# Kernel optimization log

Hardware: AMD Instinct MI355X
Metric: run time of the kernel (lower is better)

Reference implementation:

```python
import jax, jax.numpy as jnp
import numpy as np

EMBED_DIM = 768
NUM_HEADS = 12
HEAD_DIM = EMBED_DIM // NUM_HEADS
SCALE = HEAD_DIM ** -0.5


def setup_inputs() -> dict:
    key = jax.random.key(0)
    k_x, k_qw, k_qb, k_pw, k_pb = jax.random.split(key, 5)
    B, N, C = 8, 1024, EMBED_DIM
    std = C ** -0.5
    return {
        "x": jax.random.normal(k_x, (B, N, C), dtype=jnp.float32),
        "qkv_w": jax.random.normal(k_qw, (C, 3 * C), dtype=jnp.float32) * std,
        "qkv_b": jax.random.normal(k_qb, (3 * C,), dtype=jnp.float32) * 0.02,
        "proj_w": jax.random.normal(k_pw, (C, C), dtype=jnp.float32) * std,
        "proj_b": jax.random.normal(k_pb, (C,), dtype=jnp.float32) * 0.02,
    }


def reference(x, qkv_w, qkv_b, proj_w, proj_b):
    B, N, C = x.shape
    # QKV projection: [B,N,3C] -> [3,B,H,N,Dh]
    qkv = (x @ qkv_w + qkv_b).reshape(B, N, 3, NUM_HEADS, HEAD_DIM)
    qkv = jnp.transpose(qkv, (2, 0, 3, 1, 4))
    q, k, v = qkv[0], qkv[1], qkv[2]
    # attention scores [B,H,N,N]
    attn = jnp.einsum("bhqd,bhkd->bhqk", q, k) * SCALE
    attn_weights = jax.nn.softmax(attn, axis=-1)
    # dropout=0.0 (eval) -> identity
    out = jnp.einsum("bhqk,bhkd->bhqd", attn_weights, v)
    out = jnp.transpose(out, (0, 2, 1, 3)).reshape(B, N, C)
    out = out @ proj_w + proj_b
    return out, attn_weights
```

## Files before the change

### kernel.cpp

```cpp
#include <hip/hip_runtime.h>
#include <cstdint>
#include <cstddef>

namespace {

constexpr int B = 8, NSEQ = 1024, C = 768, H = 12, D = 64, N3 = 2304;
constexpr float SCALE = 0.125f;
constexpr size_t QKV_ELEMS = (size_t)B * H * NSEQ * D;

using f32x4 = __attribute__((ext_vector_type(4))) float;
using s16x8 = __attribute__((ext_vector_type(8))) short;

__device__ __forceinline__ unsigned short f2bf(float f) {
  union { float f; uint32_t u; } v; v.f = f;
  const uint32_t r = v.u + 0x7FFFu + ((v.u >> 16) & 1u);
  return (unsigned short)(r >> 16);
}
__device__ __forceinline__ float bf2f(unsigned short s) {
  union { uint32_t u; float f; } v; v.u = ((uint32_t)s) << 16;
  return v.f;
}
__device__ __forceinline__ void gload_lds16(const void* g, void* l) {
  __builtin_amdgcn_global_load_lds(
      (const __attribute__((address_space(1))) uint32_t*)g,
      (__attribute__((address_space(3))) uint32_t*)l, 16, 0, 0);
}

__global__ __launch_bounds__(256)
void cvt_x(const float* __restrict__ x, unsigned short* __restrict__ xb, int n4) {
  const int stride = gridDim.x * 256;
  for (int idx = blockIdx.x * 256 + threadIdx.x; idx < n4; idx += stride) {
    const float4 v = ((const float4*)x)[idx];
    ushort4 o;
    o.x = f2bf(v.x); o.y = f2bf(v.y); o.z = f2bf(v.z); o.w = f2bf(v.w);
    ((ushort4*)xb)[idx] = o;
  }
}

__global__ __launch_bounds__(256)
void transp_cvt(const float* __restrict__ w, unsigned short* __restrict__ wt,
                int K, int N) {
  __shared__ float t[32][33];
  const int n0 = blockIdx.x << 5, k0 = blockIdx.y << 5;
  const int tid = threadIdx.x;
  #pragma unroll
  for (int r = 0; r < 4; ++r) {
    const int e = (r << 8) + tid;
    const int kk = e >> 5, nn = e & 31;
    t[kk][nn] = w[(size_t)(k0 + kk) * N + n0 + nn];
  }
  __syncthreads();
  #pragma unroll
  for (int r = 0; r < 4; ++r) {
    const int e = (r << 8) + tid;
    const int nn = e >> 5, kk = e & 31;
    wt[(size_t)(n0 + nn) * K + k0 + kk] = f2bf(t[kk][nn]);
  }
}

template<int MODE>
__global__ __launch_bounds__(256, 2)
void gemm_bf16(const unsigned short* __restrict__ A,
               const unsigned short* __restrict__ Wt,
               const float* __restrict__ bias,
               unsigned short* __restrict__ qp, unsigned short* __restrict__ kp,
               unsigned short* __restrict__ vt, float* __restrict__ out32,
               int N, int NT) {
  constexpr int K = 768;
  __shared__ short As[128 * 64];
  __shared__ short Bs[128 * 64];
  const int tid = threadIdx.x;
  const int wid = tid >> 6, lane = tid & 63;
  const int wm = wid >> 1, wn = wid & 1;
  const int lg = lane >> 4, lr = lane & 15;

  const int cpx = gridDim.x >> 3;
  const int logical = (blockIdx.x & 7) * cpx + (blockIdx.x >> 3);
  const int bx = logical % NT, by = logical / NT;
  const int m0 = by << 7, n0 = bx << 7;

  f32x4 acc[4][4] = {};

  for (int k0 = 0; k0 < K; k0 += 64) {
    __syncthreads();
    #pragma unroll
    for (int r = 0; r < 4; ++r) {
      const int c = (r << 8) + tid;
      const int row = c >> 3, g8 = c & 7;
      const int gp = g8 ^ (row & 7);
      const int ldsoff = (((r << 8) + (wid << 6)) << 3);
      gload_lds16(A + (size_t)(m0 + row) * K + k0 + (gp << 3), (void*)(As + ldsoff));
      gload_lds16(Wt + (size_t)(n0 + row) * K + k0 + (gp << 3), (void*)(Bs + ldsoff));
    }
    __syncthreads();
    #pragma unroll
    for (int kc = 0; kc < 2; ++kc) {
      s16x8 af[4], bf[4];
      #pragma unroll
      for (int i = 0; i < 4; ++i) {
        const int ra = (wm << 6) + (i << 4) + lr;
        const int ca = ((kc << 2) + lg) ^ (ra & 7);
        af[i] = *(const s16x8*)(As + (ra << 6) + (ca << 3));
        const int rb = (wn << 6) + (i << 4) + lr;
        const int cb = ((kc << 2) + lg) ^ (rb & 7);
        bf[i] = *(const s16x8*)(Bs + (rb << 6) + (cb << 3));
      }
      #pragma unroll
      for (int i = 0; i < 4; ++i)
        #pragma unroll
        for (int j = 0; j < 4; ++j)
          acc[i][j] = __builtin_amdgcn_mfma_f32_16x16x32_bf16(af[i], bf[j], acc[i][j], 0, 0, 0);
    }
  }

  #pragma unroll
  for (int i = 0; i < 4; ++i) {
    const int m = m0 + (wm << 6) + (i << 4) + (lg << 2);
    #pragma unroll
    for (int j = 0; j < 4; ++j) {
      const int n = n0 + (wn << 6) + (j << 4) + lr;
      const float bv = bias[n];
      if (MODE == 0) {
        const int which = (n >= 1536) ? 2 : (n >= 768 ? 1 : 0);
        const int hh = (n - which * 768) >> 6;
        const int d = n & 63;
        const int b = m >> 10, ns = m & 1023;
        const size_t bh = (size_t)b * H + hh;
        if (which < 2) {
          unsigned short* dst = (which == 0 ? qp : kp) + (bh * NSEQ + ns) * D + d;
          #pragma unroll
          for (int rg = 0; rg < 4; ++rg)
            dst[(size_t)rg * D] = f2bf(acc[i][j][rg] + bv);
        } else {
          ushort4 pk;
          pk.x = f2bf(acc[i][j][0] + bv);
          pk.y = f2bf(acc[i][j][1] + bv);
          pk.z = f2bf(acc[i][j][2] + bv);
          pk.w = f2bf(acc[i][j][3] + bv);
          *(ushort4*)(vt + (bh * D + d) * NSEQ + ns) = pk;
        }
      } else {
        float* dst = out32 + (size_t)m * N + n;
        #pragma unroll
        for (int rg = 0; rg < 4; ++rg)
          dst[(size_t)rg * N] = acc[i][j][rg] + bv;
      }
    }
  }
}

constexpr int RS = 1032;

__device__ __forceinline__ int scidx(int q, int col) {
  return q * RS + ((((col >> 3) ^ (q & 7)) << 3) | (col & 7));
}

__global__ __launch_bounds__(512, 4)
void attn_mfma(const unsigned short* __restrict__ qg,
               const unsigned short* __restrict__ kg,
               const unsigned short* __restrict__ vtg,
               float* __restrict__ attnw,
               unsigned short* __restrict__ aout) {
  __shared__ __align__(16) short sc[32 * RS];
  __shared__ float invs[32];
  const int tid = threadIdx.x;
  const int wid = tid >> 6, lane = tid & 63;
  const int lg = lane >> 4, lr = lane & 15;
  const int wq = wid >> 2, ws = wid & 3;

  const int logical = (blockIdx.x & 7) * 384 + (blockIdx.x >> 3);
  const int bh = logical >> 5;
  const int q0 = (logical & 31) << 5;
  const size_t kvbase = (size_t)bh * NSEQ * D;

  s16x8 qf[2];
  #pragma unroll
  for (int kc = 0; kc < 2; ++kc)
    qf[kc] = *(const s16x8*)(qg + kvbase + (size_t)(q0 + (wq << 4) + lr) * D + (kc << 5) + (lg << 3));

  {
    const unsigned short* kptr = kg + kvbase + (size_t)((ws << 4) + lr) * D + (lg << 3);
    const int qloc = (wq << 4) + lr;
    #pragma unroll 4
    for (int t = 0; t < 16; ++t) {
      f32x4 acc = {};
      #pragma unroll
      for (int kc = 0; kc < 2; ++kc) {
        const s16x8 kf = *(const s16x8*)(kptr + t * 64 * D + (kc << 5));
        acc = __builtin_amdgcn_mfma_f32_16x16x32_bf16(kf, qf[kc], acc, 0, 0, 0);
      }
      ushort4 pk;
      pk.x = f2bf(acc[0] * SCALE); pk.y = f2bf(acc[1] * SCALE);
      pk.z = f2bf(acc[2] * SCALE); pk.w = f2bf(acc[3] * SCALE);
      *(ushort4*)(sc + scidx(qloc, (t << 6) + (ws << 4) + (lg << 2))) = pk;
    }
  }
  __syncthreads();

  {
    const int row = tid >> 4, ql = tid & 15;
    const int rx = row & 7;
    float mx = -3.0e38f;
    #pragma unroll
    for (int c = 0; c < 8; ++c) {
      const s16x8 v = *(const s16x8*)(sc + row * RS + (((ql + (c << 4)) ^ rx) << 3));
      #pragma unroll
      for (int e = 0; e < 8; ++e) mx = fmaxf(mx, bf2f((unsigned short)v[e]));
    }
    #pragma unroll
    for (int off = 8; off > 0; off >>= 1) mx = fmaxf(mx, __shfl_xor(mx, off, 16));
    float s = 0.f;
    #pragma unroll
    for (int c = 0; c < 8; ++c) {
      s16x8 v = *(s16x8*)(sc + row * RS + (((ql + (c << 4)) ^ rx) << 3));
      #pragma unroll
      for (int e = 0; e < 8; ++e) {
        const float ev = __expf(bf2f((unsigned short)v[e]) - mx);
        s += ev;
        v[e] = (short)f2bf(ev);
      }
      *(s16x8*)(sc + row * RS + (((ql + (c << 4)) ^ rx) << 3)) = v;
    }
    #pragma unroll
    for (int off = 8; off > 0; off >>= 1) s += __shfl_xor(s, off, 16);
    if (ql == 0) invs[row] = 1.0f / s;
  }
  __syncthreads();

  f32x4 oa0 = {}, oa1 = {};
  {
    const int qrow = (wq << 4) + lr;
    const int srow = tid >> 4;
    const float sinv = invs[srow];
    const unsigned short* vptr = vtg + ((size_t)bh * D + (ws << 4) + lr) * NSEQ + (lg << 3);
    float* wrow = attnw + ((size_t)bh * NSEQ + q0 + srow) * NSEQ;
    const int qx = qrow & 7;

    for (int t = 0; t < 16; ++t) {
      const int j0 = t << 6;
      #pragma unroll
      for (int kc = 0; kc < 2; ++kc) {
        const s16x8 pa = *(const s16x8*)(sc + qrow * RS + ((((j0 >> 3) + (kc << 2) + lg) ^ qx) << 3));
        const s16x8 vf = *(const s16x8*)(vptr + j0 + (kc << 5));
        if (kc == 0) oa0 = __builtin_amdgcn_mfma_f32_16x16x32_bf16(pa, vf, oa0, 0, 0, 0);
        else         oa1 = __builtin_amdgcn_mfma_f32_16x16x32_bf16(pa, vf, oa1, 0, 0, 0);
      }
      const int scol = j0 + ((tid & 15) << 2);
      const ushort4 e4 = *(const ushort4*)(sc + srow * RS + ((((scol >> 3) ^ (srow & 7)) << 3) | (scol & 7)));
      f32x4 w;
      w[0] = bf2f(e4.x) * sinv; w[1] = bf2f(e4.y) * sinv;
      w[2] = bf2f(e4.z) * sinv; w[3] = bf2f(e4.w) * sinv;
      *(f32x4*)(wrow + scol) = w;
    }
  }

  {
    const int b = bh / H, hh = bh - b * H;
    const int d = (ws << 4) + lr;
    #pragma unroll
    for (int rg = 0; rg < 4; ++rg) {
      const int qi = (wq << 4) + (lg << 2) + rg;
      aout[((size_t)b * NSEQ + q0 + qi) * C + hh * D + d] =
          f2bf((oa0[rg] + oa1[rg]) * invs[qi]);
    }
  }
}

}

extern "C" void kernel_launch(void* const* d_in, const int* in_sizes, int n_in,
                              void* d_out, int out_size, void* d_ws, size_t ws_size,
                              hipStream_t stream) {
  const float* x      = (const float*)d_in[0];
  const float* qkv_w  = (const float*)d_in[1];
  const float* qkv_b  = (const float*)d_in[2];
  const float* proj_w = (const float*)d_in[3];
  const float* proj_b = (const float*)d_in[4];

  float* out   = (float*)d_out;
  float* attnw = out + (size_t)B * NSEQ * C;

  unsigned short* xb   = (unsigned short*)d_ws;
  unsigned short* wtq  = xb   + (size_t)8192 * 768;
  unsigned short* wtp  = wtq  + (size_t)2304 * 768;
  unsigned short* qp   = wtp  + (size_t)768 * 768;
  unsigned short* kp   = qp   + QKV_ELEMS;
  unsigned short* vtp  = kp   + QKV_ELEMS;
  unsigned short* wsao = vtp  + QKV_ELEMS;

  cvt_x<<<1024, 256, 0, stream>>>(x, xb, (int)((size_t)8192 * 768 / 4));
  transp_cvt<<<dim3(N3 / 32, C / 32), 256, 0, stream>>>(qkv_w, wtq, C, N3);
  transp_cvt<<<dim3(C / 32, C / 32), 256, 0, stream>>>(proj_w, wtp, C, C);

  gemm_bf16<0><<<(N3 / 128) * (8192 / 128), 256, 0, stream>>>(
      xb, wtq, qkv_b, qp, kp, vtp, nullptr, N3, N3 / 128);

  attn_mfma<<<(NSEQ / 32) * (B * H), 512, 0, stream>>>(qp, kp, vtp, attnw, wsao);

  gemm_bf16<1><<<(C / 128) * (8192 / 128), 256, 0, stream>>>(
      wsao, wtp, proj_b, nullptr, nullptr, nullptr, out, C, C / 128);
}
```

Before: 283.2 us.

## Shrink attention blocks to 16 query rows and split weight store from PV loop

```diff
diff --git a/kernel.cpp b/kernel.cpp
--- a/kernel.cpp
+++ b/kernel.cpp
@@ -155,32 +155,30 @@
   return q * RS + ((((col >> 3) ^ (q & 7)) << 3) | (col & 7));
 }
 
-__global__ __launch_bounds__(512, 4)
+__global__ __launch_bounds__(256, 4)
 void attn_mfma(const unsigned short* __restrict__ qg,
                const unsigned short* __restrict__ kg,
                const unsigned short* __restrict__ vtg,
                float* __restrict__ attnw,
                unsigned short* __restrict__ aout) {
-  __shared__ __align__(16) short sc[32 * RS];
-  __shared__ float invs[32];
+  __shared__ __align__(16) short sc[16 * RS];
+  __shared__ float invs[16];
   const int tid = threadIdx.x;
   const int wid = tid >> 6, lane = tid & 63;
   const int lg = lane >> 4, lr = lane & 15;
-  const int wq = wid >> 2, ws = wid & 3;
-
-  const int logical = (blockIdx.x & 7) * 384 + (blockIdx.x >> 3);
-  const int bh = logical >> 5;
-  const int q0 = (logical & 31) << 5;
+
+  const int logical = (blockIdx.x & 7) * 768 + (blockIdx.x >> 3);
+  const int bh = logical >> 6;
+  const int q0 = (logical & 63) << 4;
   const size_t kvbase = (size_t)bh * NSEQ * D;
 
   s16x8 qf[2];
   #pragma unroll
   for (int kc = 0; kc < 2; ++kc)
-    qf[kc] = *(const s16x8*)(qg + kvbase + (size_t)(q0 + (wq << 4) + lr) * D + (kc << 5) + (lg << 3));
-
-  {
-    const unsigned short* kptr = kg + kvbase + (size_t)((ws << 4) + lr) * D + (lg << 3);
-    const int qloc = (wq << 4) + lr;
+    qf[kc] = *(const s16x8*)(qg + kvbase + (size_t)(q0 + lr) * D + (kc << 5) + (lg << 3));
+
+  {
+    const unsigned short* kptr = kg + kvbase + (size_t)((wid << 4) + lr) * D + (lg << 3);
     #pragma unroll 4
     for (int t = 0; t < 16; ++t) {
       f32x4 acc = {};
@@ -192,7 +190,7 @@
       ushort4 pk;
       pk.x = f2bf(acc[0] * SCALE); pk.y = f2bf(acc[1] * SCALE);
       pk.z = f2bf(acc[2] * SCALE); pk.w = f2bf(acc[3] * SCALE);
-      *(ushort4*)(sc + scidx(qloc, (t << 6) + (ws << 4) + (lg << 2))) = pk;
+      *(ushort4*)(sc + scidx(lr, (t << 6) + (wid << 4) + (lg << 2))) = pk;
     }
   }
   __syncthreads();
@@ -227,25 +225,13 @@
   }
   __syncthreads();
 
-  f32x4 oa0 = {}, oa1 = {};
-  {
-    const int qrow = (wq << 4) + lr;
+  {
     const int srow = tid >> 4;
     const float sinv = invs[srow];
-    const unsigned short* vptr = vtg + ((size_t)bh * D + (ws << 4) + lr) * NSEQ + (lg << 3);
     float* wrow = attnw + ((size_t)bh * NSEQ + q0 + srow) * NSEQ;
-    const int qx = qrow & 7;
-
-    for (int t = 0; t < 16; ++t) {
-      const int j0 = t << 6;
-      #pragma unroll
-      for (int kc = 0; kc < 2; ++kc) {
-        const s16x8 pa = *(const s16x8*)(sc + qrow * RS + ((((j0 >> 3) + (kc << 2) + lg) ^ qx) << 3));
-        const s16x8 vf = *(const s16x8*)(vptr + j0 + (kc << 5));
-        if (kc == 0) oa0 = __builtin_amdgcn_mfma_f32_16x16x32_bf16(pa, vf, oa0, 0, 0, 0);
-        else         oa1 = __builtin_amdgcn_mfma_f32_16x16x32_bf16(pa, vf, oa1, 0, 0, 0);
-      }
-      const int scol = j0 + ((tid & 15) << 2);
+    #pragma unroll 4
+    for (int c = 0; c < 16; ++c) {
+      const int scol = (c << 6) + ((tid & 15) << 2);
       const ushort4 e4 = *(const ushort4*)(sc + srow * RS + ((((scol >> 3) ^ (srow & 7)) << 3) | (scol & 7)));
       f32x4 w;
       w[0] = bf2f(e4.x) * sinv; w[1] = bf2f(e4.y) * sinv;
@@ -254,12 +240,28 @@
     }
   }
 
+  f32x4 oa0 = {}, oa1 = {};
+  {
+    const int qx = lr & 7;
+    const unsigned short* vptr = vtg + ((size_t)bh * D + (wid << 4) + lr) * NSEQ + (lg << 3);
+    #pragma unroll 2
+    for (int t = 0; t < 16; ++t) {
+      const int j0 = t << 6;
+      const s16x8 pa0 = *(const s16x8*)(sc + lr * RS + ((((j0 >> 3) + lg) ^ qx) << 3));
+      const s16x8 vf0 = *(const s16x8*)(vptr + j0);
+      oa0 = __builtin_amdgcn_mfma_f32_16x16x32_bf16(pa0, vf0, oa0, 0, 0, 0);
+      const s16x8 pa1 = *(const s16x8*)(sc + lr * RS + ((((j0 >> 3) + 4 + lg) ^ qx) << 3));
+      const s16x8 vf1 = *(const s16x8*)(vptr + j0 + 32);
+      oa1 = __builtin_amdgcn_mfma_f32_16x16x32_bf16(pa1, vf1, oa1, 0, 0, 0);
+    }
+  }
+
   {
     const int b = bh / H, hh = bh - b * H;
-    const int d = (ws << 4) + lr;
+    const int d = (wid << 4) + lr;
     #pragma unroll
     for (int rg = 0; rg < 4; ++rg) {
-      const int qi = (wq << 4) + (lg << 2) + rg;
+      const int qi = (lg << 2) + rg;
       aout[((size_t)b * NSEQ + q0 + qi) * C + hh * D + d] =
           f2bf((oa0[rg] + oa1[rg]) * invs[qi]);
     }
@@ -295,7 +297,7 @@
   gemm_bf16<0><<<(N3 / 128) * (8192 / 128), 256, 0, stream>>>(
       xb, wtq, qkv_b, qp, kp, vtp, nullptr, N3, N3 / 128);
 
-  attn_mfma<<<(NSEQ / 32) * (B * H), 512, 0, stream>>>(qp, kp, vtp, attnw, wsao);
+  attn_mfma<<<(NSEQ / 16) * (B * H), 256, 0, stream>>>(qp, kp, vtp, attnw, wsao);
 
   gemm_bf16<1><<<(C / 128) * (8192 / 128), 256, 0, stream>>>(
       wsao, wtp, proj_b, nullptr, nullptr, nullptr, out, C, C / 128);
```

After: 281.0 us. No clear change (-0.7%).
